# Kernel optimization log

Measured on AMD Instinct MI355X. Metric: run time of the kernel, lower is better.

The kernel has to match this reference:

```python
import jax, jax.numpy as jnp
import numpy as np


def setup_inputs() -> dict:
    key = jax.random.key(0)
    k1, k2, k3 = jax.random.split(key, 3)
    T, N, D = 128, 2048, 256  # snapshots, nodes, nhid
    inputs = jax.random.normal(k1, (T, N, D), dtype=jnp.float32)
    # torch init: uniform_(-0.1, 0.1)
    weight_W = jax.random.uniform(k2, (D, D), dtype=jnp.float32, minval=-0.1, maxval=0.1)
    weight_proj = jax.random.uniform(k3, (D, 1), dtype=jnp.float32, minval=-0.1, maxval=0.1)
    return {"inputs": inputs, "weight_W": weight_W, "weight_proj": weight_proj,
            "attention_width": 3}


def reference(inputs, weight_W, weight_proj, attention_width):
    # inputs: (T, N, D). For i < w the slice passes through unchanged.
    # For i >= w: window = inputs[i-w:i] (excludes position i),
    #   u = tanh(window @ W)            -> (w, N, D)
    #   a = (u @ proj).squeeze(-1)      -> (w, N)
    #   a = softmax over dim=1 (NODES)  -- legacy nn.Softmax() on 2D input
    #   out_i = sum_w a[...,None] * window -> (N, D)
    T, N, D = inputs.shape
    w = attention_width
    # windows for positions i = w .. T-1: (T-w, w, N, D)
    idx = jnp.arange(T - w)[:, None] + jnp.arange(w)[None, :]
    wins = inputs[idx]
    u = jnp.tanh(jnp.einsum('twnd,de->twne', wins, weight_W))  # (T-w, w, N, D)
    a = jnp.einsum('twnd,d->twn', u, weight_proj[:, 0])        # (T-w, w, N)
    a = jax.nn.softmax(a, axis=2)  # softmax across nodes (faithful to nn.Softmax())
    out = jnp.einsum('twn,twnd->tnd', a, wins)                 # (T-w, N, D)
    return jnp.concatenate([inputs[:w], out], axis=0)          # (T, N, D)
```

## Files before the change

kernel.cpp:

```cpp
#include <hip/hip_runtime.h>
#include <hip/hip_bf16.h>


#define T_DIM 128
#define N_DIM 2048
#define D_DIM 256
#define TS 127
#define M_TOT (TS * N_DIM)

typedef __attribute__((ext_vector_type(8))) short bf16x8;
typedef __attribute__((ext_vector_type(4))) float f32x4;

__device__ inline short f2bf(float f) {
  union { float f; unsigned u; } v; v.f = f;
  unsigned r = v.u + 0x7FFFu + ((v.u >> 16) & 1u);
  return (short)(r >> 16);
}

__global__ __launch_bounds__(256) void prep_kernel(const float* __restrict__ W,
                                                   short* __restrict__ Wt) {
  int id = blockIdx.x * 256 + threadIdx.x;
  int d = id >> 8;
  int e = id & 255;
  Wt[e * 256 + d] = f2bf(W[d * 256 + e]);
}

#define BM 128
#define BE 128
#define BK 32
#define LDSP 40

__global__ __launch_bounds__(256) void gemm_s_kernel(const float* __restrict__ x,
                                                     const short* __restrict__ Wt,
                                                     const float* __restrict__ proj,
                                                     float* __restrict__ s) {
  __shared__ short As[BM * LDSP];
  __shared__ short Bs[BE * LDSP];
  __shared__ float sred[BM][2];

  const int tid = threadIdx.x;
  const int m0 = blockIdx.x * BM;
  const int e0 = blockIdx.y * BE;
  const int lane = tid & 63;
  const int w = tid >> 6;
  const int quad = lane >> 4;
  const int l15 = lane & 15;
  const int wr = (w >> 1) * 64;
  const int we = (w & 1) * 64;

  f32x4 acc[4][4] = {};

  for (int kk = 0; kk < D_DIM; kk += BK) {
    __syncthreads();
#pragma unroll
    for (int it = 0; it < 4; ++it) {
      int slot = tid + it * 256;
      int row = slot >> 3, f4 = slot & 7;
      const float4 v = *(const float4*)(x + (size_t)(m0 + row) * D_DIM + kk + f4 * 4);
      short4 b;
      b.x = f2bf(v.x); b.y = f2bf(v.y); b.z = f2bf(v.z); b.w = f2bf(v.w);
      *(short4*)(As + row * LDSP + f4 * 4) = b;
    }
#pragma unroll
    for (int it = 0; it < 2; ++it) {
      int slot = tid + it * 256;
      int row = slot >> 2, seg = slot & 3;
      uint4 v = *(const uint4*)(Wt + (size_t)(e0 + row) * D_DIM + kk + seg * 8);
      *(uint4*)(Bs + row * LDSP + seg * 8) = v;
    }
    __syncthreads();

    bf16x8 a[4], b[4];
#pragma unroll
    for (int i = 0; i < 4; ++i)
      a[i] = *(const bf16x8*)(As + (wr + i * 16 + l15) * LDSP + quad * 8);
#pragma unroll
    for (int j = 0; j < 4; ++j)
      b[j] = *(const bf16x8*)(Bs + (we + j * 16 + l15) * LDSP + quad * 8);
#pragma unroll
    for (int i = 0; i < 4; ++i)
#pragma unroll
      for (int j = 0; j < 4; ++j)
        acc[i][j] = __builtin_amdgcn_mfma_f32_16x16x32_bf16(a[i], b[j], acc[i][j], 0, 0, 0);
  }

  float pj[4];
#pragma unroll
  for (int j = 0; j < 4; ++j) pj[j] = proj[e0 + we + j * 16 + l15];

#pragma unroll
  for (int i = 0; i < 4; ++i) {
#pragma unroll
    for (int r = 0; r < 4; ++r) {
      float val = 0.f;
#pragma unroll
      for (int j = 0; j < 4; ++j) val += tanhf(acc[i][j][r]) * pj[j];
#pragma unroll
      for (int off = 1; off < 16; off <<= 1) val += __shfl_xor(val, off);
      if (l15 == 0) sred[wr + i * 16 + quad * 4 + r][w & 1] = val;
    }
  }
  __syncthreads();
  if (tid < BM) atomicAdd(&s[m0 + tid], sred[tid][0] + sred[tid][1]);
}

__global__ __launch_bounds__(256) void softmax_kernel(const float* __restrict__ s,
                                                      float* __restrict__ p) {
  const int t = blockIdx.x;
  const int tid = threadIdx.x;
  const float* row = s + (size_t)t * N_DIM;
  float v[8];
  float mx = -1e30f;
#pragma unroll
  for (int k = 0; k < 8; ++k) {
    v[k] = row[tid + k * 256];
    mx = fmaxf(mx, v[k]);
  }
#pragma unroll
  for (int off = 1; off < 64; off <<= 1) mx = fmaxf(mx, __shfl_xor(mx, off));
  __shared__ float redm[4];
  if ((tid & 63) == 0) redm[tid >> 6] = mx;
  __syncthreads();
  mx = fmaxf(fmaxf(redm[0], redm[1]), fmaxf(redm[2], redm[3]));

  float sum = 0.f;
#pragma unroll
  for (int k = 0; k < 8; ++k) {
    v[k] = __expf(v[k] - mx);
    sum += v[k];
  }
#pragma unroll
  for (int off = 1; off < 64; off <<= 1) sum += __shfl_xor(sum, off);
  __shared__ float reds[4];
  if ((tid & 63) == 0) reds[tid >> 6] = sum;
  __syncthreads();
  sum = reds[0] + reds[1] + reds[2] + reds[3];
  float inv = 1.0f / sum;
#pragma unroll
  for (int k = 0; k < 8; ++k) p[(size_t)t * N_DIM + tid + k * 256] = v[k] * inv;
}

__global__ __launch_bounds__(256) void out_kernel(const float* __restrict__ x,
                                                  const float* __restrict__ p,
                                                  float* __restrict__ out) {
  const int gid = blockIdx.x * 256 + threadIdx.x;
  const int n = gid >> 6;
  const int d4 = gid & 63;
  const size_t base = (size_t)n * D_DIM + d4 * 4;
  const size_t tstride = (size_t)N_DIM * D_DIM;

  float4 x0 = {}, x1 = {}, x2 = {};
  float p0 = 0.f, p1 = 0.f, p2 = 0.f;
  for (int t = 0; t < T_DIM; ++t) {
    const float4 xc = *(const float4*)(x + t * tstride + base);
    const float pc = (t < TS) ? p[(size_t)t * N_DIM + n] : 0.f;
    float4 o;
    if (t >= 3) {
      o.x = p0 * x0.x + p1 * x1.x + p2 * x2.x;
      o.y = p0 * x0.y + p1 * x1.y + p2 * x2.y;
      o.z = p0 * x0.z + p1 * x1.z + p2 * x2.z;
      o.w = p0 * x0.w + p1 * x1.w + p2 * x2.w;
    } else {
      o = xc;
    }
    *(float4*)(out + t * tstride + base) = o;
    x0 = x1; x1 = x2; x2 = xc;
    p0 = p1; p1 = p2; p2 = pc;
  }
}

extern "C" void kernel_launch(void* const* d_in, const int* in_sizes, int n_in,
                              void* d_out, int out_size, void* d_ws, size_t ws_size,
                              hipStream_t stream) {
  const float* x = (const float*)d_in[0];
  const float* W = (const float*)d_in[1];
  const float* proj = (const float*)d_in[2];
  float* out = (float*)d_out;

  char* ws = (char*)d_ws;
  short* Wt = (short*)ws;
  float* s = (float*)(ws + 131072);
  float* p = (float*)(ws + 131072 + 1040384);

  hipLaunchKernelGGL(prep_kernel, dim3(256), dim3(256), 0, stream, W, Wt);
  hipMemsetAsync(s, 0, (size_t)M_TOT * sizeof(float), stream);

  hipLaunchKernelGGL(gemm_s_kernel, dim3(M_TOT / BM, D_DIM / BE), dim3(256), 0, stream,
                     x, Wt, proj, s);

  hipLaunchKernelGGL(softmax_kernel, dim3(TS), dim3(256), 0, stream, s, p);

  hipLaunchKernelGGL(out_kernel, dim3((N_DIM * 64) / 256), dim3(256), 0, stream,
                     x, p, out);
}
```

Before: 581.7 us.

## Restructure GEMM to full-E tiles with register-prefetched A and split out kernel over time

The GEMM kernel now computes all 256 output columns per block (BM=256, 512 threads). A is converted from registers with double-buffered prefetch and W is staged in swizzled LDS in two halves. This removes the second E-tile pass over x, the atomics and the memset. tanh is replaced by an exp-based fast approximation. The output kernel is split over time chunks of 32 to expose more parallelism, at the cost of reloading three halo snapshots per chunk.

After: 542.3 us. 6.8% less time.

```diff
diff --git a/kernel.cpp b/kernel.cpp
--- a/kernel.cpp
+++ b/kernel.cpp
@@ -7,6 +7,8 @@
 #define D_DIM 256
 #define TS 127
 #define M_TOT (TS * N_DIM)
+#define BM 256
+#define TB 32
 
 typedef __attribute__((ext_vector_type(8))) short bf16x8;
 typedef __attribute__((ext_vector_type(4))) float f32x4;
@@ -15,6 +17,18 @@
   union { float f; unsigned u; } v; v.f = f;
   unsigned r = v.u + 0x7FFFu + ((v.u >> 16) & 1u);
   return (short)(r >> 16);
+}
+
+__device__ inline bf16x8 cvt8(const float4 a, const float4 b) {
+  bf16x8 r;
+  r[0] = f2bf(a.x); r[1] = f2bf(a.y); r[2] = f2bf(a.z); r[3] = f2bf(a.w);
+  r[4] = f2bf(b.x); r[5] = f2bf(b.y); r[6] = f2bf(b.z); r[7] = f2bf(b.w);
+  return r;
+}
+
+__device__ inline float fast_tanh(float x) {
+  float e = __expf(fminf(2.0f * x, 30.0f));
+  return __fdividef(e - 1.0f, e + 1.0f);
 }
 
 __global__ __launch_bounds__(256) void prep_kernel(const float* __restrict__ W,
@@ -25,83 +39,101 @@
   Wt[e * 256 + d] = f2bf(W[d * 256 + e]);
 }
 
-#define BM 128
-#define BE 128
-#define BK 32
-#define LDSP 40
-
-__global__ __launch_bounds__(256) void gemm_s_kernel(const float* __restrict__ x,
+__global__ __launch_bounds__(512) void gemm_s_kernel(const float* __restrict__ x,
                                                      const short* __restrict__ Wt,
                                                      const float* __restrict__ proj,
                                                      float* __restrict__ s) {
-  __shared__ short As[BM * LDSP];
-  __shared__ short Bs[BE * LDSP];
-  __shared__ float sred[BM][2];
+  __shared__ short Ws[256 * 128];
 
   const int tid = threadIdx.x;
-  const int m0 = blockIdx.x * BM;
-  const int e0 = blockIdx.y * BE;
   const int lane = tid & 63;
   const int w = tid >> 6;
   const int quad = lane >> 4;
   const int l15 = lane & 15;
-  const int wr = (w >> 1) * 64;
-  const int we = (w & 1) * 64;
-
-  f32x4 acc[4][4] = {};
-
-  for (int kk = 0; kk < D_DIM; kk += BK) {
+  const int m0 = blockIdx.x * BM;
+  const size_t row0 = (size_t)(m0 + w * 32 + l15);
+  const float* xp = x + row0 * D_DIM + quad * 8;
+  const int swzc = (l15 & 7) << 4;
+
+  float4 A0[2][2], A1[2][2];
+  A0[0][0] = *(const float4*)(xp);
+  A0[0][1] = *(const float4*)(xp + 4);
+  A0[1][0] = *(const float4*)(xp + 16 * D_DIM);
+  A0[1][1] = *(const float4*)(xp + 16 * D_DIM + 4);
+  A1[0][0] = *(const float4*)(xp + 32);
+  A1[0][1] = *(const float4*)(xp + 36);
+  A1[1][0] = *(const float4*)(xp + 32 + 16 * D_DIM);
+  A1[1][1] = *(const float4*)(xp + 36 + 16 * D_DIM);
+
+  f32x4 acc[2][16] = {};
+
+#pragma unroll
+  for (int half = 0; half < 2; ++half) {
+    if (half) __syncthreads();
+#pragma unroll
+    for (int it = 0; it < 8; ++it) {
+      int slot = tid + it * 512;
+      int e = slot >> 4;
+      int ks = slot & 15;
+      uint4 v = *(const uint4*)(Wt + e * D_DIM + half * 128 + ks * 8);
+      int dst = (e * 256 + ks * 16) ^ ((e & 7) << 4);
+      *(uint4*)((char*)Ws + dst) = v;
+    }
     __syncthreads();
-#pragma unroll
-    for (int it = 0; it < 4; ++it) {
-      int slot = tid + it * 256;
-      int row = slot >> 3, f4 = slot & 7;
-      const float4 v = *(const float4*)(x + (size_t)(m0 + row) * D_DIM + kk + f4 * 4);
-      short4 b;
-      b.x = f2bf(v.x); b.y = f2bf(v.y); b.z = f2bf(v.z); b.w = f2bf(v.w);
-      *(short4*)(As + row * LDSP + f4 * 4) = b;
-    }
-#pragma unroll
-    for (int it = 0; it < 2; ++it) {
-      int slot = tid + it * 256;
-      int row = slot >> 2, seg = slot & 3;
-      uint4 v = *(const uint4*)(Wt + (size_t)(e0 + row) * D_DIM + kk + seg * 8);
-      *(uint4*)(Bs + row * LDSP + seg * 8) = v;
-    }
-    __syncthreads();
-
-    bf16x8 a[4], b[4];
-#pragma unroll
-    for (int i = 0; i < 4; ++i)
-      a[i] = *(const bf16x8*)(As + (wr + i * 16 + l15) * LDSP + quad * 8);
-#pragma unroll
-    for (int j = 0; j < 4; ++j)
-      b[j] = *(const bf16x8*)(Bs + (we + j * 16 + l15) * LDSP + quad * 8);
-#pragma unroll
-    for (int i = 0; i < 4; ++i)
-#pragma unroll
-      for (int j = 0; j < 4; ++j)
-        acc[i][j] = __builtin_amdgcn_mfma_f32_16x16x32_bf16(a[i], b[j], acc[i][j], 0, 0, 0);
-  }
-
-  float pj[4];
-#pragma unroll
-  for (int j = 0; j < 4; ++j) pj[j] = proj[e0 + we + j * 16 + l15];
-
-#pragma unroll
-  for (int i = 0; i < 4; ++i) {
+
+#pragma unroll
+    for (int kt = 0; kt < 4; ++kt) {
+      const int kg = half * 4 + kt;
+      bf16x8 a0, a1;
+      if ((kg & 1) == 0) {
+        a0 = cvt8(A0[0][0], A0[0][1]);
+        a1 = cvt8(A0[1][0], A0[1][1]);
+        if (kg < 6) {
+          const float* q = xp + (kg + 2) * 32;
+          A0[0][0] = *(const float4*)(q);
+          A0[0][1] = *(const float4*)(q + 4);
+          A0[1][0] = *(const float4*)(q + 16 * D_DIM);
+          A0[1][1] = *(const float4*)(q + 16 * D_DIM + 4);
+        }
+      } else {
+        a0 = cvt8(A1[0][0], A1[0][1]);
+        a1 = cvt8(A1[1][0], A1[1][1]);
+        if (kg < 6) {
+          const float* q = xp + (kg + 2) * 32;
+          A1[0][0] = *(const float4*)(q);
+          A1[0][1] = *(const float4*)(q + 4);
+          A1[1][0] = *(const float4*)(q + 16 * D_DIM);
+          A1[1][1] = *(const float4*)(q + 16 * D_DIM + 4);
+        }
+      }
+      const int kb = (kt * 64 + quad * 16) ^ swzc;
+#pragma unroll
+      for (int ef = 0; ef < 16; ++ef) {
+        const bf16x8 b =
+            *(const bf16x8*)((const char*)Ws + (ef * 16 + l15) * 256 + kb);
+        acc[0][ef] = __builtin_amdgcn_mfma_f32_16x16x32_bf16(a0, b, acc[0][ef], 0, 0, 0);
+        acc[1][ef] = __builtin_amdgcn_mfma_f32_16x16x32_bf16(a1, b, acc[1][ef], 0, 0, 0);
+      }
+    }
+  }
+
+  float pj[16];
+#pragma unroll
+  for (int ef = 0; ef < 16; ++ef) pj[ef] = proj[ef * 16 + l15];
+
+#pragma unroll
+  for (int mf = 0; mf < 2; ++mf) {
 #pragma unroll
     for (int r = 0; r < 4; ++r) {
       float val = 0.f;
 #pragma unroll
-      for (int j = 0; j < 4; ++j) val += tanhf(acc[i][j][r]) * pj[j];
+      for (int ef = 0; ef < 16; ++ef)
+        val = __builtin_fmaf(fast_tanh(acc[mf][ef][r]), pj[ef], val);
 #pragma unroll
       for (int off = 1; off < 16; off <<= 1) val += __shfl_xor(val, off);
-      if (l15 == 0) sred[wr + i * 16 + quad * 4 + r][w & 1] = val;
-    }
-  }
-  __syncthreads();
-  if (tid < BM) atomicAdd(&s[m0 + tid], sred[tid][0] + sred[tid][1]);
+      if (l15 == 0) s[m0 + w * 32 + mf * 16 + quad * 4 + r] = val;
+    }
+  }
 }
 
 __global__ __launch_bounds__(256) void softmax_kernel(const float* __restrict__ s,
@@ -146,12 +178,21 @@
   const int gid = blockIdx.x * 256 + threadIdx.x;
   const int n = gid >> 6;
   const int d4 = gid & 63;
+  const int t0 = blockIdx.y * TB;
   const size_t base = (size_t)n * D_DIM + d4 * 4;
   const size_t tstride = (size_t)N_DIM * D_DIM;
 
   float4 x0 = {}, x1 = {}, x2 = {};
   float p0 = 0.f, p1 = 0.f, p2 = 0.f;
-  for (int t = 0; t < T_DIM; ++t) {
+  if (t0 >= 3) {
+    x0 = *(const float4*)(x + (t0 - 3) * tstride + base);
+    x1 = *(const float4*)(x + (t0 - 2) * tstride + base);
+    x2 = *(const float4*)(x + (t0 - 1) * tstride + base);
+    p0 = p[(size_t)(t0 - 3) * N_DIM + n];
+    p1 = p[(size_t)(t0 - 2) * N_DIM + n];
+    p2 = p[(size_t)(t0 - 1) * N_DIM + n];
+  }
+  for (int t = t0; t < t0 + TB; ++t) {
     const float4 xc = *(const float4*)(x + t * tstride + base);
     const float pc = (t < TS) ? p[(size_t)t * N_DIM + n] : 0.f;
     float4 o;
@@ -183,13 +224,12 @@
   float* p = (float*)(ws + 131072 + 1040384);
 
   hipLaunchKernelGGL(prep_kernel, dim3(256), dim3(256), 0, stream, W, Wt);
-  hipMemsetAsync(s, 0, (size_t)M_TOT * sizeof(float), stream);
-
-  hipLaunchKernelGGL(gemm_s_kernel, dim3(M_TOT / BM, D_DIM / BE), dim3(256), 0, stream,
+
+  hipLaunchKernelGGL(gemm_s_kernel, dim3(M_TOT / BM), dim3(512), 0, stream,
                      x, Wt, proj, s);
 
   hipLaunchKernelGGL(softmax_kernel, dim3(TS), dim3(256), 0, stream, s, p);
 
-  hipLaunchKernelGGL(out_kernel, dim3((N_DIM * 64) / 256), dim3(256), 0, stream,
-                     x, p, out);
-}
+  hipLaunchKernelGGL(out_kernel, dim3((N_DIM * 64) / 256, T_DIM / TB), dim3(256), 0,
+                     stream, x, p, out);
+}
```
